# Performance work log

Measured on AMD Instinct MI355X. Metric: run time of the kernel, lower is better.

The kernel has to match this reference:

```python
import jax, jax.numpy as jnp
import numpy as np

B, S, D_MODEL = 2, 2048, 2048
N_HEADS, D_HEAD = 32, 64
SEQ_MAX = 2048


def _rope_cache(seq_len, d_head):
    half = d_head // 2
    inv_freq = 1.0 / (10000.0 ** (np.arange(0, half, dtype=np.float32) / half))
    t = np.arange(seq_len, dtype=np.float32)
    freqs = np.einsum('i,j->ij', t, inv_freq)  # [S, half]
    emb = np.concatenate([freqs, freqs], axis=-1)  # [S, d_head]
    return jnp.asarray(np.cos(emb)), jnp.asarray(np.sin(emb))


def _rotate_half(x):
    half = x.shape[-1] // 2
    return jnp.concatenate([-x[..., half:], x[..., :half]], axis=-1)


def setup_inputs() -> dict:
    key = jax.random.key(0)
    ks = jax.random.split(key, 9)
    std = 0.02
    mk = lambda k: jax.random.normal(k, (D_MODEL, D_MODEL), jnp.float32) * std
    return {
        'x': jax.random.normal(ks[0], (B, S, D_MODEL), jnp.float32),
        'Wq': mk(ks[1]), 'bq': jnp.zeros((D_MODEL,), jnp.float32),
        'Wk': mk(ks[2]), 'bk': jnp.zeros((D_MODEL,), jnp.float32),
        'Wv': mk(ks[3]), 'bv': jnp.zeros((D_MODEL,), jnp.float32),
        'Wo': mk(ks[4]), 'bo': jnp.zeros((D_MODEL,), jnp.float32),
    }


def reference(x, Wq, bq, Wk, bk, Wv, bv, Wo, bo):
    Bsz, S_len, _ = x.shape
    # projections (torch Linear: y = x @ W^T + b)
    q = x @ Wq.T + bq
    k = x @ Wk.T + bk
    v = x @ Wv.T + bv
    # [B, H, S, Dh]
    to_heads = lambda t: t.reshape(Bsz, S_len, N_HEADS, D_HEAD).transpose(0, 2, 1, 3)
    q, k, v = to_heads(q), to_heads(k), to_heads(v)
    cos, sin = _rope_cache(S_len, D_HEAD)  # [S, Dh]
    cos = cos[None, None]
    sin = sin[None, None]
    q = q * cos + _rotate_half(q) * sin
    k = k * cos + _rotate_half(k) * sin
    scale = 1.0 / jnp.sqrt(jnp.float32(D_HEAD))
    att = jnp.einsum('bhqd,bhkd->bhqk', q, k) * scale
    causal = jnp.tril(jnp.ones((S_len, S_len), dtype=bool))
    att = jnp.where(causal[None, None], att, jnp.float32(-jnp.inf))
    att = jax.nn.softmax(att, axis=-1)
    # sigmoid-gated values (dropout = identity at inference)
    y = jnp.einsum('bhqk,bhkd->bhqd', att, jax.nn.sigmoid(v))
    y = y.transpose(0, 2, 1, 3).reshape(Bsz, S_len, D_MODEL)
    return y @ Wo.T + bo
```

## Files before the change

kernel.cpp:

```cpp
#include <hip/hip_runtime.h>

typedef unsigned short u16;
typedef float f32x4 __attribute__((ext_vector_type(4)));
typedef __bf16 bf16x8 __attribute__((ext_vector_type(8)));

#define S_LEN 2048
#define DM 2048
#define NHEAD 32
#define DHEAD 64

__device__ __forceinline__ u16 f2bf(float f) {
    __bf16 b = (__bf16)f;
    return __builtin_bit_cast(u16, b);
}
__device__ __forceinline__ float bf2f(u16 u) {
    return (float)__builtin_bit_cast(__bf16, u);
}
__device__ __forceinline__ void async16(const void* g, void* l) {
    __builtin_amdgcn_global_load_lds(
        (const __attribute__((address_space(1))) unsigned int*)g,
        (__attribute__((address_space(3))) unsigned int*)l, 16, 0, 0);
}

__global__ __launch_bounds__(256) void cast_kernel(const float* __restrict__ in,
                                                   u16* __restrict__ out, long long n) {
    long long i = ((long long)blockIdx.x * 256 + threadIdx.x) * 4;
    if (i + 3 < n) {
        float4 f = *(const float4*)(in + i);
        ushort4 v;
        v.x = f2bf(f.x); v.y = f2bf(f.y); v.z = f2bf(f.z); v.w = f2bf(f.w);
        *(ushort4*)(out + i) = v;
    }
}

__global__ __launch_bounds__(256) void gemm_qkv(const u16* __restrict__ A,
                                                const u16* __restrict__ Bt,
                                                const float* __restrict__ bq,
                                                const float* __restrict__ bk,
                                                const float* __restrict__ bv,
                                                u16* __restrict__ Qo, u16* __restrict__ Ko,
                                                u16* __restrict__ VTo, int M, int K) {
    __shared__ __align__(16) u16 As[128 * 32];
    __shared__ __align__(16) u16 Bs[128 * 32];
    int tid = threadIdx.x;
    int w = tid >> 6, lane = tid & 63, quad = lane >> 4, l16 = lane & 15;
    int m0 = blockIdx.x * 128;
    int n0 = blockIdx.y * 128;
    int sel = n0 >> 11;
    int nloc = n0 & 2047;
    int wm = (w & 1) * 64, wn = (w >> 1) * 64;

    f32x4 acc[4][4] = {};
    const u16* ga = A + (long long)m0 * K;
    const u16* gb = Bt + (long long)n0 * K;

    for (int k0 = 0; k0 < K; k0 += 32) {
#pragma unroll
        for (int rr = 0; rr < 2; ++rr) {
            int c = tid + rr * 256;
            int row = c >> 2, kc = c & 3;
            async16(ga + (long long)row * K + k0 + kc * 8, (char*)As + c * 16);
            async16(gb + (long long)row * K + k0 + kc * 8, (char*)Bs + c * 16);
        }
        __syncthreads();
        bf16x8 af[4], bfv[4];
#pragma unroll
        for (int mt = 0; mt < 4; ++mt)
            af[mt] = *(const bf16x8*)(As + (wm + mt * 16 + l16) * 32 + quad * 8);
#pragma unroll
        for (int nt = 0; nt < 4; ++nt)
            bfv[nt] = *(const bf16x8*)(Bs + (wn + nt * 16 + l16) * 32 + quad * 8);
#pragma unroll
        for (int mt = 0; mt < 4; ++mt)
#pragma unroll
            for (int nt = 0; nt < 4; ++nt)
                acc[mt][nt] = __builtin_amdgcn_mfma_f32_16x16x32_bf16(af[mt], bfv[nt],
                                                                      acc[mt][nt], 0, 0, 0);
        __syncthreads();
    }

    if (sel < 2) {
        float scale = sel == 0 ? 0.125f : 1.0f;
        u16* out = sel == 0 ? Qo : Ko;
        const float* bias = sel == 0 ? bq : bk;
#pragma unroll
        for (int ntl = 0; ntl < 2; ++ntl) {
            int col = nloc + wn + ntl * 16 + l16;
            int j = (wn + ntl * 16 + l16) & 63;
            float inv = __expf(-(float)j * 0.28782313662425575f);
            float ci, si;
            sincosf(inv, &si, &ci);
            float b1 = bias[col], b2 = bias[col + 32];
#pragma unroll
            for (int mt = 0; mt < 4; ++mt) {
                int rowb = m0 + wm + mt * 16 + quad * 4;
                int s0 = rowb & (S_LEN - 1);
                float sn, cs;
                sincosf((float)s0 * inv, &sn, &cs);
#pragma unroll
                for (int r = 0; r < 4; ++r) {
                    int row = rowb + r;
                    float x1 = acc[mt][ntl][r] + b1;
                    float x2 = acc[mt][ntl + 2][r] + b2;
                    out[(long long)row * 2048 + col] = f2bf((x1 * cs - x2 * sn) * scale);
                    out[(long long)row * 2048 + col + 32] = f2bf((x2 * cs + x1 * sn) * scale);
                    float c2 = cs * ci - sn * si;
                    float s2 = sn * ci + cs * si;
                    cs = c2; sn = s2;
                }
            }
        }
    } else {
#pragma unroll
        for (int mt = 0; mt < 4; ++mt) {
            int rowb = m0 + wm + mt * 16 + quad * 4;
            int b = rowb >> 11;
            int s0 = rowb & (S_LEN - 1);
#pragma unroll
            for (int nt = 0; nt < 4; ++nt) {
                int col = nloc + wn + nt * 16 + l16;
                int h = col >> 6, d = col & 63;
                float bvs = bv[col];
                ushort4 pk;
                float v0 = acc[mt][nt][0] + bvs;
                float v1 = acc[mt][nt][1] + bvs;
                float v2 = acc[mt][nt][2] + bvs;
                float v3 = acc[mt][nt][3] + bvs;
                pk.x = f2bf(1.f / (1.f + __expf(-v0)));
                pk.y = f2bf(1.f / (1.f + __expf(-v1)));
                pk.z = f2bf(1.f / (1.f + __expf(-v2)));
                pk.w = f2bf(1.f / (1.f + __expf(-v3)));
                *(ushort4*)(VTo + ((long long)((b * NHEAD + h) * DHEAD + d)) * S_LEN + s0) = pk;
            }
        }
    }
}

__global__ __launch_bounds__(256) void gemm_bt_f32(const u16* __restrict__ A,
                                                   const u16* __restrict__ Bt,
                                                   const float* __restrict__ bias,
                                                   float* __restrict__ Cout,
                                                   int M, int N, int K) {
    __shared__ __align__(16) u16 As[128 * 32];
    __shared__ __align__(16) u16 Bs[128 * 32];
    int tid = threadIdx.x;
    int w = tid >> 6, lane = tid & 63, quad = lane >> 4, l16 = lane & 15;
    int m0 = blockIdx.x * 128;
    int n0 = blockIdx.y * 128;
    int wm = (w & 1) * 64, wn = (w >> 1) * 64;

    f32x4 acc[4][4] = {};
    const u16* ga = A + (long long)m0 * K;
    const u16* gb = Bt + (long long)n0 * K;

    for (int k0 = 0; k0 < K; k0 += 32) {
#pragma unroll
        for (int rr = 0; rr < 2; ++rr) {
            int c = tid + rr * 256;
            int row = c >> 2, kc = c & 3;
            async16(ga + (long long)row * K + k0 + kc * 8, (char*)As + c * 16);
            async16(gb + (long long)row * K + k0 + kc * 8, (char*)Bs + c * 16);
        }
        __syncthreads();
        bf16x8 af[4], bfv[4];
#pragma unroll
        for (int mt = 0; mt < 4; ++mt)
            af[mt] = *(const bf16x8*)(As + (wm + mt * 16 + l16) * 32 + quad * 8);
#pragma unroll
        for (int nt = 0; nt < 4; ++nt)
            bfv[nt] = *(const bf16x8*)(Bs + (wn + nt * 16 + l16) * 32 + quad * 8);
#pragma unroll
        for (int mt = 0; mt < 4; ++mt)
#pragma unroll
            for (int nt = 0; nt < 4; ++nt)
                acc[mt][nt] = __builtin_amdgcn_mfma_f32_16x16x32_bf16(af[mt], bfv[nt],
                                                                      acc[mt][nt], 0, 0, 0);
        __syncthreads();
    }

#pragma unroll
    for (int mt = 0; mt < 4; ++mt) {
#pragma unroll
        for (int nt = 0; nt < 4; ++nt) {
            int col = n0 + wn + nt * 16 + l16;
            float bvs = bias[col];
#pragma unroll
            for (int r = 0; r < 4; ++r) {
                int row = m0 + wm + mt * 16 + quad * 4 + r;
                Cout[(long long)row * N + col] = acc[mt][nt][r] + bvs;
            }
        }
    }
}

__global__ __launch_bounds__(256, 4) void flash_attn(const u16* __restrict__ Q,
                                                     const u16* __restrict__ K,
                                                     const u16* __restrict__ VT,
                                                     u16* __restrict__ Y) {
    int bid = blockIdx.x;
    int pi = bid & 15;
    int h = (bid >> 4) & 31;
    int b = bid >> 9;
    int tid = threadIdx.x;
    int w = tid >> 6, lane = tid & 63, quad = lane >> 4, l16 = lane & 15;

    __shared__ __align__(16) u16 Kl[64 * 64];
    __shared__ __align__(16) u16 Vl[64 * 64];
    __shared__ __align__(16) u16 Pl[4][16 * 72];

    const u16* kbase = K + ((long long)(b * S_LEN)) * DM + h * DHEAD;
    const u16* vbase = VT + ((long long)((b * NHEAD + h) * DHEAD)) * S_LEN;

    bf16x8 kpre[2], vpre[2];
    int c0 = tid, c1 = tid + 256;
    int row0 = c0 >> 3, lc0 = (c0 & 7) ^ (row0 & 7);
    int row1 = c1 >> 3, lc1 = (c1 & 7) ^ (row1 & 7);

    {
        kpre[0] = *(const bf16x8*)(kbase + (long long)row0 * DM + lc0 * 8);
        vpre[0] = *(const bf16x8*)(vbase + (long long)row0 * S_LEN + lc0 * 8);
        kpre[1] = *(const bf16x8*)(kbase + (long long)row1 * DM + lc1 * 8);
        vpre[1] = *(const bf16x8*)(vbase + (long long)row1 * S_LEN + lc1 * 8);
    }

#pragma unroll 1
    for (int rep = 0; rep < 2; ++rep) {
        int qt = rep ? 31 - pi : pi;
        int qrow = qt * 64 + w * 16 + l16;
        const u16* qp = Q + ((long long)(b * S_LEN + qrow)) * DM + h * DHEAD + quad * 8;
        bf16x8 aq0 = *(const bf16x8*)(qp);
        bf16x8 aq1 = *(const bf16x8*)(qp + 32);

        f32x4 o[4] = {};
        float m_r = -__builtin_inff(), l_r = 0.f;

#pragma unroll 1
        for (int kt = 0; kt <= qt; ++kt) {
            int k0 = kt * 64;
            __syncthreads();
            *(bf16x8*)((char*)Kl + c0 * 16) = kpre[0];
            *(bf16x8*)((char*)Vl + c0 * 16) = vpre[0];
            *(bf16x8*)((char*)Kl + c1 * 16) = kpre[1];
            *(bf16x8*)((char*)Vl + c1 * 16) = vpre[1];
            {
                int nk0 = (kt < qt ? kt + 1 : 0) * 64;
                kpre[0] = *(const bf16x8*)(kbase + (long long)(nk0 + row0) * DM + lc0 * 8);
                vpre[0] = *(const bf16x8*)(vbase + (long long)row0 * S_LEN + nk0 + lc0 * 8);
                kpre[1] = *(const bf16x8*)(kbase + (long long)(nk0 + row1) * DM + lc1 * 8);
                vpre[1] = *(const bf16x8*)(vbase + (long long)row1 * S_LEN + nk0 + lc1 * 8);
            }
            __syncthreads();

            f32x4 s[4];
#pragma unroll
            for (int nt = 0; nt < 4; ++nt) {
                int row = nt * 16 + l16;
                int sw0 = (quad ^ (row & 7)) * 8;
                int sw1 = ((quad + 4) ^ (row & 7)) * 8;
                bf16x8 ak0 = *(const bf16x8*)(Kl + row * 64 + sw0);
                bf16x8 ak1 = *(const bf16x8*)(Kl + row * 64 + sw1);
                f32x4 a = {};
                a = __builtin_amdgcn_mfma_f32_16x16x32_bf16(ak0, aq0, a, 0, 0, 0);
                a = __builtin_amdgcn_mfma_f32_16x16x32_bf16(ak1, aq1, a, 0, 0, 0);
                s[nt] = a;
            }
            if (kt == qt) {
                int qg = qt * 64 + w * 16 + l16;
#pragma unroll
                for (int nt = 0; nt < 4; ++nt) {
#pragma unroll
                    for (int r = 0; r < 4; ++r) {
                        int kc = k0 + nt * 16 + quad * 4 + r;
                        if (kc > qg) s[nt][r] = -__builtin_inff();
                    }
                }
            }
            float mx = s[0][0];
#pragma unroll
            for (int nt = 0; nt < 4; ++nt)
#pragma unroll
                for (int r = 0; r < 4; ++r) mx = fmaxf(mx, s[nt][r]);
            mx = fmaxf(mx, __shfl_xor(mx, 16, 64));
            mx = fmaxf(mx, __shfl_xor(mx, 32, 64));
            float mnew = fmaxf(m_r, mx);
            float alpha = __expf(m_r - mnew);
            m_r = mnew;
#pragma unroll
            for (int nt = 0; nt < 4; ++nt)
#pragma unroll
                for (int r = 0; r < 4; ++r) s[nt][r] = __expf(s[nt][r] - mnew);
            float sum = 0.f;
#pragma unroll
            for (int nt = 0; nt < 4; ++nt)
#pragma unroll
                for (int r = 0; r < 4; ++r) sum += s[nt][r];
            sum += __shfl_xor(sum, 16, 64);
            sum += __shfl_xor(sum, 32, 64);
            l_r = l_r * alpha + sum;

#pragma unroll
            for (int dt = 0; dt < 4; ++dt)
#pragma unroll
                for (int r = 0; r < 4; ++r) o[dt][r] *= alpha;

            u16* pw = &Pl[w][0];
#pragma unroll
            for (int nt = 0; nt < 4; ++nt) {
                ushort4 pk;
                pk.x = f2bf(s[nt][0]); pk.y = f2bf(s[nt][1]);
                pk.z = f2bf(s[nt][2]); pk.w = f2bf(s[nt][3]);
                *(ushort4*)(pw + l16 * 72 + nt * 16 + quad * 4) = pk;
            }
            bf16x8 bp0 = *(const bf16x8*)(pw + l16 * 72 + quad * 8);
            bf16x8 bp1 = *(const bf16x8*)(pw + l16 * 72 + 32 + quad * 8);
#pragma unroll
            for (int dt = 0; dt < 4; ++dt) {
                int row = dt * 16 + l16;
                int sw0 = (quad ^ (row & 7)) * 8;
                int sw1 = ((quad + 4) ^ (row & 7)) * 8;
                bf16x8 av0 = *(const bf16x8*)(Vl + row * 64 + sw0);
                bf16x8 av1 = *(const bf16x8*)(Vl + row * 64 + sw1);
                o[dt] = __builtin_amdgcn_mfma_f32_16x16x32_bf16(av0, bp0, o[dt], 0, 0, 0);
                o[dt] = __builtin_amdgcn_mfma_f32_16x16x32_bf16(av1, bp1, o[dt], 0, 0, 0);
            }
        }

        float inv_l = 1.f / l_r;
        u16* yp = Y + ((long long)(b * S_LEN + qt * 64 + w * 16 + l16)) * DM + h * DHEAD;
#pragma unroll
        for (int dt = 0; dt < 4; ++dt) {
            ushort4 yk;
            yk.x = f2bf(o[dt][0] * inv_l);
            yk.y = f2bf(o[dt][1] * inv_l);
            yk.z = f2bf(o[dt][2] * inv_l);
            yk.w = f2bf(o[dt][3] * inv_l);
            *(ushort4*)(yp + dt * 16 + quad * 4) = yk;
        }
    }
}

extern "C" void kernel_launch(void* const* d_in, const int* in_sizes, int n_in,
                              void* d_out, int out_size, void* d_ws, size_t ws_size,
                              hipStream_t stream) {
    const float* x  = (const float*)d_in[0];
    const float* Wq = (const float*)d_in[1];
    const float* bq = (const float*)d_in[2];
    const float* Wk = (const float*)d_in[3];
    const float* bk = (const float*)d_in[4];
    const float* Wv = (const float*)d_in[5];
    const float* bv = (const float*)d_in[6];
    const float* Wo = (const float*)d_in[7];
    const float* bo = (const float*)d_in[8];

    const long long M = 2LL * S_LEN;
    const long long NX = M * DM;
    const long long NW = (long long)DM * DM;

    char* ws = (char*)d_ws;
    u16* xb   = (u16*)(ws);
    u16* Wqkv = (u16*)(ws + 16 * 1024 * 1024);
    u16* Wob  = (u16*)(ws + 40 * 1024 * 1024);
    u16* Qb   = (u16*)(ws + 48 * 1024 * 1024);
    u16* Kb   = (u16*)(ws + 64 * 1024 * 1024);
    u16* VTb  = (u16*)(ws + 80 * 1024 * 1024);
    u16* Yb   = (u16*)(ws + 96 * 1024 * 1024);

    cast_kernel<<<(int)(NX / 1024), 256, 0, stream>>>(x, xb, NX);
    cast_kernel<<<(int)(NW / 1024), 256, 0, stream>>>(Wq, Wqkv, NW);
    cast_kernel<<<(int)(NW / 1024), 256, 0, stream>>>(Wk, Wqkv + NW, NW);
    cast_kernel<<<(int)(NW / 1024), 256, 0, stream>>>(Wv, Wqkv + 2 * NW, NW);
    cast_kernel<<<(int)(NW / 1024), 256, 0, stream>>>(Wo, Wob, NW);

    dim3 gqkv(32, 48);
    gemm_qkv<<<gqkv, 256, 0, stream>>>(xb, Wqkv, bq, bk, bv, Qb, Kb, VTb, (int)M, DM);

    flash_attn<<<2 * NHEAD * 16, 256, 0, stream>>>(Qb, Kb, VTb, Yb);

    dim3 gg(32, 16);
    gemm_bt_f32<<<gg, 256, 0, stream>>>(Yb, Wob, bo, (float*)d_out, (int)M, DM, DM);
}
```

Baseline: 459.0 us.

## Fuse cast kernels, double-buffer attention K/V tiles, use exp2 and fast sincos

The five cast launches become one kernel that picks its source tensor by block index. Flash attention now double-buffers the K/V LDS tiles, which removes the per-iteration barrier before the stores, and swizzles the P scratch buffer instead of padding it. The softmax switches to hardware exp2 by folding log2(e) into the Q scale. The RoPE sincos calls use hardware sin/cos with range reduction, and the frequency index is simplified. Removing the barrier relies on double buffering and per-wave ordering to stay race-free, and the hardware transcendentals may lose some accuracy.

Result: no change. 452.9 us (-1.3%).

```diff
diff --git a/kernel.cpp b/kernel.cpp
--- a/kernel.cpp
+++ b/kernel.cpp
@@ -13,24 +13,41 @@
     __bf16 b = (__bf16)f;
     return __builtin_bit_cast(u16, b);
 }
-__device__ __forceinline__ float bf2f(u16 u) {
-    return (float)__builtin_bit_cast(__bf16, u);
-}
 __device__ __forceinline__ void async16(const void* g, void* l) {
     __builtin_amdgcn_global_load_lds(
         (const __attribute__((address_space(1))) unsigned int*)g,
         (__attribute__((address_space(3))) unsigned int*)l, 16, 0, 0);
 }
-
-__global__ __launch_bounds__(256) void cast_kernel(const float* __restrict__ in,
-                                                   u16* __restrict__ out, long long n) {
-    long long i = ((long long)blockIdx.x * 256 + threadIdx.x) * 4;
-    if (i + 3 < n) {
-        float4 f = *(const float4*)(in + i);
-        ushort4 v;
-        v.x = f2bf(f.x); v.y = f2bf(f.y); v.z = f2bf(f.z); v.w = f2bf(f.w);
-        *(ushort4*)(out + i) = v;
-    }
+__device__ __forceinline__ void fast_sincos(float th, float* s, float* c) {
+    float rev = th * 0.15915494309189535f;
+    rev = rev - floorf(rev);
+    *s = __builtin_amdgcn_sinf(rev);
+    *c = __builtin_amdgcn_cosf(rev);
+}
+__device__ __forceinline__ float fexp2(float x) { return __builtin_amdgcn_exp2f(x); }
+
+__global__ __launch_bounds__(256) void cast_all(const float* __restrict__ x,
+                                                const float* __restrict__ Wq,
+                                                const float* __restrict__ Wk,
+                                                const float* __restrict__ Wv,
+                                                const float* __restrict__ Wo,
+                                                u16* __restrict__ xb,
+                                                u16* __restrict__ Wqkv,
+                                                u16* __restrict__ Wob) {
+    int bid = blockIdx.x;
+    const float* src;
+    u16* dst;
+    long long off;
+    if (bid < 8192)       { src = x;  dst = xb;             off = (long long)bid * 1024; }
+    else if (bid < 12288) { src = Wq; dst = Wqkv;           off = (long long)(bid - 8192) * 1024; }
+    else if (bid < 16384) { src = Wk; dst = Wqkv + 4194304; off = (long long)(bid - 12288) * 1024; }
+    else if (bid < 20480) { src = Wv; dst = Wqkv + 8388608; off = (long long)(bid - 16384) * 1024; }
+    else                  { src = Wo; dst = Wob;            off = (long long)(bid - 20480) * 1024; }
+    long long i = off + threadIdx.x * 4;
+    float4 f = *(const float4*)(src + i);
+    ushort4 v;
+    v.x = f2bf(f.x); v.y = f2bf(f.y); v.z = f2bf(f.z); v.w = f2bf(f.w);
+    *(ushort4*)(dst + i) = v;
 }
 
 __global__ __launch_bounds__(256) void gemm_qkv(const u16* __restrict__ A,
@@ -80,23 +97,23 @@
     }
 
     if (sel < 2) {
-        float scale = sel == 0 ? 0.125f : 1.0f;
+        float scale = sel == 0 ? 0.18033688011112042f : 1.0f;
         u16* out = sel == 0 ? Qo : Ko;
         const float* bias = sel == 0 ? bq : bk;
 #pragma unroll
         for (int ntl = 0; ntl < 2; ++ntl) {
             int col = nloc + wn + ntl * 16 + l16;
-            int j = (wn + ntl * 16 + l16) & 63;
+            int j = (ntl * 16 + l16) & 31;
             float inv = __expf(-(float)j * 0.28782313662425575f);
             float ci, si;
-            sincosf(inv, &si, &ci);
+            fast_sincos(inv, &si, &ci);
             float b1 = bias[col], b2 = bias[col + 32];
 #pragma unroll
             for (int mt = 0; mt < 4; ++mt) {
                 int rowb = m0 + wm + mt * 16 + quad * 4;
                 int s0 = rowb & (S_LEN - 1);
                 float sn, cs;
-                sincosf((float)s0 * inv, &sn, &cs);
+                fast_sincos((float)s0 * inv, &sn, &cs);
 #pragma unroll
                 for (int r = 0; r < 4; ++r) {
                     int row = rowb + r;
@@ -122,14 +139,10 @@
                 int h = col >> 6, d = col & 63;
                 float bvs = bv[col];
                 ushort4 pk;
-                float v0 = acc[mt][nt][0] + bvs;
-                float v1 = acc[mt][nt][1] + bvs;
-                float v2 = acc[mt][nt][2] + bvs;
-                float v3 = acc[mt][nt][3] + bvs;
-                pk.x = f2bf(1.f / (1.f + __expf(-v0)));
-                pk.y = f2bf(1.f / (1.f + __expf(-v1)));
-                pk.z = f2bf(1.f / (1.f + __expf(-v2)));
-                pk.w = f2bf(1.f / (1.f + __expf(-v3)));
+                pk.x = f2bf(1.f / (1.f + __expf(-(acc[mt][nt][0] + bvs))));
+                pk.y = f2bf(1.f / (1.f + __expf(-(acc[mt][nt][1] + bvs))));
+                pk.z = f2bf(1.f / (1.f + __expf(-(acc[mt][nt][2] + bvs))));
+                pk.w = f2bf(1.f / (1.f + __expf(-(acc[mt][nt][3] + bvs))));
                 *(ushort4*)(VTo + ((long long)((b * NHEAD + h) * DHEAD + d)) * S_LEN + s0) = pk;
             }
         }
@@ -204,9 +217,9 @@
     int tid = threadIdx.x;
     int w = tid >> 6, lane = tid & 63, quad = lane >> 4, l16 = lane & 15;
 
-    __shared__ __align__(16) u16 Kl[64 * 64];
-    __shared__ __align__(16) u16 Vl[64 * 64];
-    __shared__ __align__(16) u16 Pl[4][16 * 72];
+    __shared__ __align__(16) u16 Kl[2][64 * 64];
+    __shared__ __align__(16) u16 Vl[2][64 * 64];
+    __shared__ __align__(16) u16 Pl[4][16 * 64];
 
     const u16* kbase = K + ((long long)(b * S_LEN)) * DM + h * DHEAD;
     const u16* vbase = VT + ((long long)((b * NHEAD + h) * DHEAD)) * S_LEN;
@@ -216,13 +229,12 @@
     int row0 = c0 >> 3, lc0 = (c0 & 7) ^ (row0 & 7);
     int row1 = c1 >> 3, lc1 = (c1 & 7) ^ (row1 & 7);
 
-    {
-        kpre[0] = *(const bf16x8*)(kbase + (long long)row0 * DM + lc0 * 8);
-        vpre[0] = *(const bf16x8*)(vbase + (long long)row0 * S_LEN + lc0 * 8);
-        kpre[1] = *(const bf16x8*)(kbase + (long long)row1 * DM + lc1 * 8);
-        vpre[1] = *(const bf16x8*)(vbase + (long long)row1 * S_LEN + lc1 * 8);
-    }
-
+    kpre[0] = *(const bf16x8*)(kbase + (long long)row0 * DM + lc0 * 8);
+    vpre[0] = *(const bf16x8*)(vbase + (long long)row0 * S_LEN + lc0 * 8);
+    kpre[1] = *(const bf16x8*)(kbase + (long long)row1 * DM + lc1 * 8);
+    vpre[1] = *(const bf16x8*)(vbase + (long long)row1 * S_LEN + lc1 * 8);
+
+    int it = 0;
 #pragma unroll 1
     for (int rep = 0; rep < 2; ++rep) {
         int qt = rep ? 31 - pi : pi;
@@ -237,11 +249,12 @@
 #pragma unroll 1
         for (int kt = 0; kt <= qt; ++kt) {
             int k0 = kt * 64;
-            __syncthreads();
-            *(bf16x8*)((char*)Kl + c0 * 16) = kpre[0];
-            *(bf16x8*)((char*)Vl + c0 * 16) = vpre[0];
-            *(bf16x8*)((char*)Kl + c1 * 16) = kpre[1];
-            *(bf16x8*)((char*)Vl + c1 * 16) = vpre[1];
+            u16* Kb_ = Kl[it & 1];
+            u16* Vb_ = Vl[it & 1];
+            *(bf16x8*)((char*)Kb_ + c0 * 16) = kpre[0];
+            *(bf16x8*)((char*)Vb_ + c0 * 16) = vpre[0];
+            *(bf16x8*)((char*)Kb_ + c1 * 16) = kpre[1];
+            *(bf16x8*)((char*)Vb_ + c1 * 16) = vpre[1];
             {
                 int nk0 = (kt < qt ? kt + 1 : 0) * 64;
                 kpre[0] = *(const bf16x8*)(kbase + (long long)(nk0 + row0) * DM + lc0 * 8);
@@ -257,8 +270,8 @@
                 int row = nt * 16 + l16;
                 int sw0 = (quad ^ (row & 7)) * 8;
                 int sw1 = ((quad + 4) ^ (row & 7)) * 8;
-                bf16x8 ak0 = *(const bf16x8*)(Kl + row * 64 + sw0);
-                bf16x8 ak1 = *(const bf16x8*)(Kl + row * 64 + sw1);
+                bf16x8 ak0 = *(const bf16x8*)(Kb_ + row * 64 + sw0);
+                bf16x8 ak1 = *(const bf16x8*)(Kb_ + row * 64 + sw1);
                 f32x4 a = {};
                 a = __builtin_amdgcn_mfma_f32_16x16x32_bf16(ak0, aq0, a, 0, 0, 0);
                 a = __builtin_amdgcn_mfma_f32_16x16x32_bf16(ak1, aq1, a, 0, 0, 0);
@@ -283,12 +296,12 @@
             mx = fmaxf(mx, __shfl_xor(mx, 16, 64));
             mx = fmaxf(mx, __shfl_xor(mx, 32, 64));
             float mnew = fmaxf(m_r, mx);
-            float alpha = __expf(m_r - mnew);
+            float alpha = fexp2(m_r - mnew);
             m_r = mnew;
 #pragma unroll
             for (int nt = 0; nt < 4; ++nt)
 #pragma unroll
-                for (int r = 0; r < 4; ++r) s[nt][r] = __expf(s[nt][r] - mnew);
+                for (int r = 0; r < 4; ++r) s[nt][r] = fexp2(s[nt][r] - mnew);
             float sum = 0.f;
 #pragma unroll
             for (int nt = 0; nt < 4; ++nt)
@@ -309,20 +322,22 @@
                 ushort4 pk;
                 pk.x = f2bf(s[nt][0]); pk.y = f2bf(s[nt][1]);
                 pk.z = f2bf(s[nt][2]); pk.w = f2bf(s[nt][3]);
-                *(ushort4*)(pw + l16 * 72 + nt * 16 + quad * 4) = pk;
-            }
-            bf16x8 bp0 = *(const bf16x8*)(pw + l16 * 72 + quad * 8);
-            bf16x8 bp1 = *(const bf16x8*)(pw + l16 * 72 + 32 + quad * 8);
+                int chunk = (nt * 2 + (quad >> 1)) ^ (l16 & 7);
+                *(ushort4*)(pw + l16 * 64 + chunk * 8 + (quad & 1) * 4) = pk;
+            }
+            bf16x8 bp0 = *(const bf16x8*)(pw + l16 * 64 + (quad ^ (l16 & 7)) * 8);
+            bf16x8 bp1 = *(const bf16x8*)(pw + l16 * 64 + ((quad + 4) ^ (l16 & 7)) * 8);
 #pragma unroll
             for (int dt = 0; dt < 4; ++dt) {
                 int row = dt * 16 + l16;
                 int sw0 = (quad ^ (row & 7)) * 8;
                 int sw1 = ((quad + 4) ^ (row & 7)) * 8;
-                bf16x8 av0 = *(const bf16x8*)(Vl + row * 64 + sw0);
-                bf16x8 av1 = *(const bf16x8*)(Vl + row * 64 + sw1);
+                bf16x8 av0 = *(const bf16x8*)(Vb_ + row * 64 + sw0);
+                bf16x8 av1 = *(const bf16x8*)(Vb_ + row * 64 + sw1);
                 o[dt] = __builtin_amdgcn_mfma_f32_16x16x32_bf16(av0, bp0, o[dt], 0, 0, 0);
                 o[dt] = __builtin_amdgcn_mfma_f32_16x16x32_bf16(av1, bp1, o[dt], 0, 0, 0);
             }
+            ++it;
         }
 
         float inv_l = 1.f / l_r;
@@ -353,8 +368,6 @@
     const float* bo = (const float*)d_in[8];
 
     const long long M = 2LL * S_LEN;
-    const long long NX = M * DM;
-    const long long NW = (long long)DM * DM;
 
     char* ws = (char*)d_ws;
     u16* xb   = (u16*)(ws);
@@ -365,11 +378,7 @@
     u16* VTb  = (u16*)(ws + 80 * 1024 * 1024);
     u16* Yb   = (u16*)(ws + 96 * 1024 * 1024);
 
-    cast_kernel<<<(int)(NX / 1024), 256, 0, stream>>>(x, xb, NX);
-    cast_kernel<<<(int)(NW / 1024), 256, 0, stream>>>(Wq, Wqkv, NW);
-    cast_kernel<<<(int)(NW / 1024), 256, 0, stream>>>(Wk, Wqkv + NW, NW);
-    cast_kernel<<<(int)(NW / 1024), 256, 0, stream>>>(Wv, Wqkv + 2 * NW, NW);
-    cast_kernel<<<(int)(NW / 1024), 256, 0, stream>>>(Wo, Wob, NW);
+    cast_all<<<24576, 256, 0, stream>>>(x, Wq, Wk, Wv, Wo, xb, Wqkv, Wob);
 
     dim3 gqkv(32, 48);
     gemm_qkv<<<gqkv, 256, 0, stream>>>(xb, Wqkv, bq, bk, bv, Qb, Kb, VTb, (int)M, DM);
```
